# Optimization experiments

Hardware: AMD Instinct MI355X
Metric: run time of the kernel (lower is better)

Reference implementation:

```python
import jax, jax.numpy as jnp
import numpy as np

N_HEAD = 16

def _rope_cos_sin(T, head_dim, dtype):
    # inv_freq over even indices, freqs [T, head_dim//2]
    inv_freq = 1.0 / (10000.0 ** (jnp.arange(0, head_dim, 2, dtype=jnp.float32) / head_dim))
    t = jnp.arange(T, dtype=jnp.float32)
    freqs = t[:, None] * inv_freq[None, :]
    cos = jnp.cos(freqs).astype(dtype)[None, :, None, :]  # [1,T,1,hd/2]
    sin = jnp.sin(freqs).astype(dtype)[None, :, None, :]
    return cos, sin

def _apply_rope(x, cos, sin):
    # x: [B,T,H,hd]; interleaved halves as in the torch module
    x1, x2 = x[..., ::2], x[..., 1::2]
    return jnp.concatenate([x1 * cos - x2 * sin, x1 * sin + x2 * cos], axis=-1)

def setup_inputs() -> dict:
    key = jax.random.key(0)
    k1, k2, k3 = jax.random.split(key, 3)
    B, T, C = 2, 2048, 1024
    x = jax.random.normal(k1, (B, T, C), dtype=jnp.float32)
    # causal mask (mask==0 positions get -inf), broadcast over B and heads
    attn_mask = jnp.tril(jnp.ones((T, T), dtype=bool))[None, None, :, :]
    w_qkv = jax.random.normal(k2, (C, 3 * C), dtype=jnp.float32) * (1.0 / np.sqrt(C))
    w_out = jax.random.normal(k3, (C, C), dtype=jnp.float32) * (1.0 / np.sqrt(C))
    return {"x": x, "attn_mask": attn_mask, "w_qkv": w_qkv, "w_out": w_out}

def reference(x, attn_mask, w_qkv, w_out):
    B, T, C = x.shape
    H = N_HEAD
    hd = C // H
    qkv = x @ w_qkv  # [B,T,3C]
    q, k, v = jnp.split(qkv, 3, axis=2)
    q = q.reshape(B, T, H, hd)
    k = k.reshape(B, T, H, hd)
    v = v.reshape(B, T, H, hd)
    cos, sin = _rope_cos_sin(T, hd, x.dtype)
    q = _apply_rope(q, cos, sin)
    k = _apply_rope(k, cos, sin)
    scale = 1.0 / np.sqrt(hd).astype(np.float32)
    att = jnp.einsum('bthd,bshd->bhts', q, k) * scale  # [B,H,T,T]
    att = jnp.where(attn_mask, att, -jnp.inf)
    att = jax.nn.softmax(att, axis=-1)
    out = jnp.einsum('bhts,bshd->bthd', att, v).reshape(B, T, C)
    out = out @ w_out
    k_t = jnp.transpose(k, (0, 2, 1, 3))  # [B,H,T,hd]
    v_t = jnp.transpose(v, (0, 2, 1, 3))
    return out, k_t, v_t
```

## Files before the change

### kernel.cpp

```cpp
#include <hip/hip_runtime.h>

#define T_SEQ 2048
#define NH    16
#define HD    64
#define CDIM  1024
#define BDIM  2

using floatx4 = __attribute__((ext_vector_type(4))) float;
using bf16x8  = __attribute__((ext_vector_type(8))) __bf16;
using half4   = __attribute__((ext_vector_type(4))) _Float16;
using half8   = __attribute__((ext_vector_type(8))) _Float16;
typedef unsigned short u16;

__device__ __forceinline__ u16 f2bf(float f) {
  unsigned int u = __float_as_uint(f);
  u += 0x7fffu + ((u >> 16) & 1u);
  return (u16)(u >> 16);
}
__device__ __forceinline__ float bf2f(u16 h) {
  return __uint_as_float(((unsigned int)h) << 16);
}
__device__ __forceinline__ u16 f2h(float f) {
  union { _Float16 h; u16 u; } c; c.h = (_Float16)f; return c.u;
}
__device__ __forceinline__ unsigned pk2h(float a, float b) {
  return __builtin_bit_cast(unsigned, __builtin_amdgcn_cvt_pkrtz(a, b));
}
__device__ __forceinline__ void gld16(const void* g, const void* l) {
  __builtin_amdgcn_global_load_lds(
      (const __attribute__((address_space(1))) unsigned int*)(unsigned long long)g,
      (__attribute__((address_space(3))) unsigned int*)(unsigned int)(unsigned long long)l,
      16, 0, 0);
}

__global__ __launch_bounds__(256) void preproc(const float* __restrict__ x,
                                               const float* __restrict__ w_qkv,
                                               const float* __restrict__ w_out,
                                               u16* __restrict__ xb,
                                               u16* __restrict__ wqT,
                                               u16* __restrict__ woT) {
  __shared__ float tile[32][33];
  int blk = blockIdx.x, tid = threadIdx.x;
  if (blk < 4096) {
    int i = blk * 256 + tid;
    float4 v = ((const float4*)x)[i];
    ushort4 o;
    o.x = f2bf(v.x); o.y = f2bf(v.y); o.z = f2bf(v.z); o.w = f2bf(v.w);
    ((ushort4*)xb)[i] = o;
    return;
  }
  const float* W; u16* WT; int K, N, bx, by;
  if (blk < 4096 + 3072) {
    int idx = blk - 4096; W = w_qkv; WT = wqT; K = 1024; N = 3072;
    bx = idx % 96; by = idx / 96;
  } else {
    int idx = blk - 7168; W = w_out; WT = woT; K = 1024; N = 1024;
    bx = idx & 31; by = idx >> 5;
  }
  int n0 = bx * 32, k0 = by * 32;
  int tx = tid & 31, ty = tid >> 5;
#pragma unroll
  for (int i = 0; i < 32; i += 8)
    tile[ty + i][tx] = W[(size_t)(k0 + ty + i) * N + n0 + tx];
  __syncthreads();
#pragma unroll
  for (int i = 0; i < 32; i += 8)
    WT[(size_t)(n0 + ty + i) * K + k0 + tx] = f2bf(tile[tx][ty + i]);
}

template <bool OUT_F32>
__global__ __launch_bounds__(256) void gemm_bt(const u16* __restrict__ A,
                                               const u16* __restrict__ BT,
                                               float* __restrict__ Cf,
                                               u16* __restrict__ Cb,
                                               int M, int N, int K) {
  __shared__ u16 As[2][128 * 32];
  __shared__ u16 Bs[2][128 * 32];
  const int tid  = threadIdx.x;
  const int lane = tid & 63, wave = tid >> 6;
  const int quad = lane >> 4, l16 = lane & 15;
  const int wm = (wave & 1) * 64, wn = (wave >> 1) * 64;
  const int row0 = blockIdx.x * 128, col0 = blockIdx.y * 128;
  const int srow = tid >> 2;
  const int sc   = tid & 3;
  const int sgc  = (sc ^ ((srow >> 1) & 3)) * 8;
  floatx4 acc[4][4] = {};

  auto stage = [&](int buf, int k0) {
    gld16(A  + (size_t)(row0 + srow     ) * K + k0 + sgc, &As[buf][srow * 32 + sc * 8]);
    gld16(A  + (size_t)(row0 + srow + 64) * K + k0 + sgc, &As[buf][(srow + 64) * 32 + sc * 8]);
    gld16(BT + (size_t)(col0 + srow     ) * K + k0 + sgc, &Bs[buf][srow * 32 + sc * 8]);
    gld16(BT + (size_t)(col0 + srow + 64) * K + k0 + sgc, &Bs[buf][(srow + 64) * 32 + sc * 8]);
  };

  const int nk = K >> 5;
  stage(0, 0);
  for (int ki = 0; ki < nk; ki++) {
    const int cur = ki & 1;
    __builtin_amdgcn_s_barrier();
    int kn = ki + 1 < nk ? ki + 1 : nk - 1;
    stage(cur ^ 1, kn << 5);
    asm volatile("s_waitcnt vmcnt(4)" ::: "memory");
    __builtin_amdgcn_s_barrier();
    bf16x8 af[4], bfv[4];
#pragma unroll
    for (int mt = 0; mt < 4; mt++) {
      int r = wm + mt * 16 + l16;
      af[mt] = *(const bf16x8*)&As[cur][r * 32 + (quad ^ ((r >> 1) & 3)) * 8];
    }
#pragma unroll
    for (int nt = 0; nt < 4; nt++) {
      int r = wn + nt * 16 + l16;
      bfv[nt] = *(const bf16x8*)&Bs[cur][r * 32 + (quad ^ ((r >> 1) & 3)) * 8];
    }
#pragma unroll
    for (int mt = 0; mt < 4; mt++)
#pragma unroll
      for (int nt = 0; nt < 4; nt++)
        acc[mt][nt] = __builtin_amdgcn_mfma_f32_16x16x32_bf16(af[mt], bfv[nt], acc[mt][nt], 0, 0, 0);
  }
  asm volatile("s_waitcnt vmcnt(0)" ::: "memory");
#pragma unroll
  for (int mt = 0; mt < 4; mt++)
#pragma unroll
    for (int nt = 0; nt < 4; nt++)
#pragma unroll
      for (int r = 0; r < 4; r++) {
        int row = row0 + wm + mt * 16 + quad * 4 + r;
        int col = col0 + wn + nt * 16 + l16;
        float v = acc[mt][nt][r];
        if (OUT_F32) Cf[(size_t)row * N + col] = v;
        else         Cb[(size_t)row * N + col] = f2bf(v);
      }
}

__global__ __launch_bounds__(256) void rope_vpack(const u16* __restrict__ qkv,
                                                  u16* __restrict__ qf16,
                                                  u16* __restrict__ kf16,
                                                  float* __restrict__ kt_out,
                                                  float* __restrict__ vt_out,
                                                  u16* __restrict__ vtf) {
  int blk = blockIdx.x;
  if (blk < 16384) {
    int gid = blk * 4 + (threadIdx.x >> 6);
    int d   = threadIdx.x & 63;
    int t   = gid & (T_SEQ - 1);
    int h   = (gid >> 11) & 15;
    int b   = gid >> 15;
    const u16* qrow = qkv + ((size_t)(b * T_SEQ + t)) * 3072 + h * 64;
    int i = d & 31;
    unsigned int qp = *(const unsigned int*)(qrow + 2 * i);
    unsigned int kp = *(const unsigned int*)(qrow + 1024 + 2 * i);
    float q1 = bf2f((u16)qp), q2 = bf2f((u16)(qp >> 16));
    float k1 = bf2f((u16)kp), k2 = bf2f((u16)(kp >> 16));
    float inv = expf((float)i * -0.28782313662425572f);
    float ang = (float)t * inv;
    float sn = sinf(ang), cs = cosf(ang);
    float qv = (d < 32) ? (q1 * cs - q2 * sn) : (q1 * sn + q2 * cs);
    float kv = (d < 32) ? (k1 * cs - k2 * sn) : (k1 * sn + k2 * cs);
    size_t o = (size_t)gid * 64 + d;
    qf16[o] = f2h(qv * 0.18033688011112042f);
    kf16[o] = f2h(kv);
    kt_out[o] = kv;
    return;
  }
  __shared__ float tile[64][65];
  int b2 = blk - 16384;
  int t0 = (b2 & 31) * 64;
  int bh = b2 >> 5;
  int b = bh >> 4, h = bh & 15;
  int tx = threadIdx.x & 63, ty = threadIdx.x >> 6;
#pragma unroll
  for (int i = ty; i < 64; i += 4) {
    float v = bf2f(qkv[((size_t)(b * T_SEQ + t0 + i)) * 3072 + 2048 + h * 64 + tx]);
    tile[i][tx] = v;
    vt_out[((size_t)bh * T_SEQ + t0 + i) * 64 + tx] = v;
  }
  __syncthreads();
#pragma unroll
  for (int i = ty; i < 64; i += 4)
    vtf[((size_t)bh * 64 + i) * T_SEQ + t0 + tx] = f2h(tile[tx][i]);
}

__device__ __forceinline__ void qk_dual(const u16* Ks, const half8* qfA, const half8* qfB,
                                        floatx4 (&sA)[8], floatx4 (&sB)[8],
                                        int quad, int l16) {
#pragma unroll
  for (int kc = 0; kc < 2; kc++)
#pragma unroll
    for (int st = 0; st < 8; st++) {
      int srow = st * 16 + l16;
      half8 ak = *(const half8*)&Ks[srow * 64 + (((kc * 4 + quad) ^ (srow & 7)) * 8)];
      sA[st] = __builtin_amdgcn_mfma_f32_16x16x32_f16(ak, qfA[kc], sA[st], 0, 0, 0);
      sB[st] = __builtin_amdgcn_mfma_f32_16x16x32_f16(ak, qfB[kc], sB[st], 0, 0, 0);
    }
}
__device__ __forceinline__ void qk_single(const u16* Ks, const half8* qfA,
                                          floatx4 (&sA)[8], int quad, int l16) {
#pragma unroll
  for (int kc = 0; kc < 2; kc++)
#pragma unroll
    for (int st = 0; st < 8; st++) {
      int srow = st * 16 + l16;
      half8 ak = *(const half8*)&Ks[srow * 64 + (((kc * 4 + quad) ^ (srow & 7)) * 8)];
      sA[st] = __builtin_amdgcn_mfma_f32_16x16x32_f16(ak, qfA[kc], sA[st], 0, 0, 0);
    }
}
__device__ __forceinline__ void apply_mask(floatx4 (&s)[8], int kt, int tw, int quad, int l16) {
  int tg = tw + l16;
#pragma unroll
  for (int st = 0; st < 8; st++) {
    int sg = kt * 128 + st * 16 + quad * 4;
#pragma unroll
    for (int r = 0; r < 4; r++)
      if (sg + r > tg) s[st][r] = -1e30f;
  }
}
__device__ __forceinline__ float vmax4(const floatx4& v) {
  return fmaxf(fmaxf(fmaxf(v[0], v[1]), v[2]), v[3]);
}
__device__ __forceinline__ void softmax_update(floatx4 (&s)[8], float& mrow,
                                               floatx4& lsum, floatx4 (&oacc)[4]) {
  float p0 = fmaxf(vmax4(s[0]), vmax4(s[1]));
  float p1 = fmaxf(vmax4(s[2]), vmax4(s[3]));
  float p2 = fmaxf(vmax4(s[4]), vmax4(s[5]));
  float p3 = fmaxf(vmax4(s[6]), vmax4(s[7]));
  float mx = fmaxf(fmaxf(fmaxf(p0, p1), p2), p3);
  mx = fmaxf(mx, __shfl_xor(mx, 16));
  mx = fmaxf(mx, __shfl_xor(mx, 32));
  if (!__all(mx <= mrow + 8.f)) {
    float mnew = fmaxf(mrow, mx);
    float alpha = exp2f(mrow - mnew);
    mrow = mnew;
    lsum *= alpha;
#pragma unroll
    for (int dt = 0; dt < 4; dt++) oacc[dt] *= alpha;
  }
#pragma unroll
  for (int st = 0; st < 8; st++)
#pragma unroll
    for (int r = 0; r < 4; r++) s[st][r] = exp2f(s[st][r] - mrow);
}
__device__ __forceinline__ void pv_dual(const u16* Vts, const floatx4 (&sA)[8],
                                        const floatx4 (&sB)[8], floatx4 (&oA)[4],
                                        floatx4 (&oB)[4], floatx4& lsA, floatx4& lsB,
                                        int qh2, int ql2, int l16) {
  const half4 vones = {(_Float16)1.f, (_Float16)1.f, (_Float16)1.f, (_Float16)1.f};
#pragma unroll
  for (int st = 0; st < 8; st++) {
    union { unsigned u[2]; half4 h; } pa, pb;
    pa.u[0] = pk2h(sA[st][0], sA[st][1]); pa.u[1] = pk2h(sA[st][2], sA[st][3]);
    pb.u[0] = pk2h(sB[st][0], sB[st][1]); pb.u[1] = pk2h(sB[st][2], sB[st][3]);
    lsA = __builtin_amdgcn_mfma_f32_16x16x16f16(vones, pa.h, lsA, 0, 0, 0);
    lsB = __builtin_amdgcn_mfma_f32_16x16x16f16(vones, pb.h, lsB, 0, 0, 0);
#pragma unroll
    for (int dt = 0; dt < 4; dt++) {
      int drow = dt * 16 + l16;
      half4 av = *(const half4*)&Vts[drow * 128 + (((st * 2 + qh2) ^ (drow & 15)) * 8) + ql2];
      oA[dt] = __builtin_amdgcn_mfma_f32_16x16x16f16(av, pa.h, oA[dt], 0, 0, 0);
      oB[dt] = __builtin_amdgcn_mfma_f32_16x16x16f16(av, pb.h, oB[dt], 0, 0, 0);
    }
  }
}
__device__ __forceinline__ void pv_single(const u16* Vts, const floatx4 (&sA)[8],
                                          floatx4 (&oA)[4], floatx4& lsA,
                                          int qh2, int ql2, int l16) {
  const half4 vones = {(_Float16)1.f, (_Float16)1.f, (_Float16)1.f, (_Float16)1.f};
#pragma unroll
  for (int st = 0; st < 8; st++) {
    union { unsigned u[2]; half4 h; } pa;
    pa.u[0] = pk2h(sA[st][0], sA[st][1]); pa.u[1] = pk2h(sA[st][2], sA[st][3]);
    lsA = __builtin_amdgcn_mfma_f32_16x16x16f16(vones, pa.h, lsA, 0, 0, 0);
#pragma unroll
    for (int dt = 0; dt < 4; dt++) {
      int drow = dt * 16 + l16;
      half4 av = *(const half4*)&Vts[drow * 128 + (((st * 2 + qh2) ^ (drow & 15)) * 8) + ql2];
      oA[dt] = __builtin_amdgcn_mfma_f32_16x16x16f16(av, pa.h, oA[dt], 0, 0, 0);
    }
  }
}
__device__ __forceinline__ void epilogue(u16* __restrict__ Ob, const floatx4 (&oacc)[4],
                                         const floatx4& lsum, int b, int h, int tw,
                                         int quad, int l16) {
  int t = tw + l16;
  float invl = 1.f / lsum[0];
#pragma unroll
  for (int dt = 0; dt < 4; dt++) {
    int d0 = dt * 16 + quad * 4;
    ushort4 o;
    o.x = f2bf(oacc[dt][0] * invl);
    o.y = f2bf(oacc[dt][1] * invl);
    o.z = f2bf(oacc[dt][2] * invl);
    o.w = f2bf(oacc[dt][3] * invl);
    *(ushort4*)&Ob[((size_t)(b * T_SEQ) + t) * CDIM + h * HD + d0] = o;
  }
}

__global__ __launch_bounds__(256, 2) void attn_fused(const u16* __restrict__ qf16,
                                                     const u16* __restrict__ kf16,
                                                     const u16* __restrict__ vtf,
                                                     u16* __restrict__ Ob) {
  __shared__ u16 Ks[128 * 64];
  __shared__ u16 Vts[64 * 128];
  const int tid = threadIdx.x;
  const int lane = tid & 63, wave = tid >> 6;
  const int quad = lane >> 4, l16 = lane & 15;
  const int qh2 = quad >> 1, ql2 = (quad & 1) * 4;
  const int j   = blockIdx.x >> 5;
  const int bh  = blockIdx.x & 31;
  const int b = bh >> 4, h = bh & 15;

  const int qtA = 31 - j, qtB = j;
  const int twA = qtA * 64 + wave * 16;
  const int twB = qtB * 64 + wave * 16;
  const int nktA = (qtA >> 1) + 1;
  const int nktB = (qtB >> 1) + 1;

  const u16* QgA = qf16 + ((size_t)bh * T_SEQ + twA) * HD;
  const u16* QgB = qf16 + ((size_t)bh * T_SEQ + twB) * HD;
  half8 qfA[2], qfB[2];
#pragma unroll
  for (int kc = 0; kc < 2; kc++) {
    qfA[kc] = *(const half8*)&QgA[(size_t)l16 * HD + kc * 32 + quad * 8];
    qfB[kc] = *(const half8*)&QgB[(size_t)l16 * HD + kc * 32 + quad * 8];
  }

  floatx4 oaccA[4] = {}, oaccB[4] = {};
  floatx4 lsA = {}, lsB = {};
  float mA = -1e30f, mB = -1e30f;

#pragma unroll 1
  for (int kt = 0; kt < nktA; kt++) {
    __syncthreads();
    const size_t koff = ((size_t)bh * T_SEQ + kt * 128) * HD;
    const u16* Vg = vtf + (size_t)bh * HD * T_SEQ + kt * 128;
#pragma unroll
    for (int jj = 0; jj < 4; jj++) {
      int t2 = jj * 256 + tid;
      int r = t2 >> 3, c = t2 & 7;
      gld16(kf16 + koff + r * HD + (c ^ (r & 7)) * 8, &Ks[t2 * 8]);
    }
#pragma unroll
    for (int jj = 0; jj < 4; jj++) {
      int t2 = jj * 256 + tid;
      int r = t2 >> 4, c = t2 & 15;
      gld16(Vg + (size_t)r * T_SEQ + (c ^ (r & 15)) * 8, &Vts[t2 * 8]);
    }
    __syncthreads();

    if (kt < nktB) {
      floatx4 sA[8] = {}, sB[8] = {};
      qk_dual(Ks, qfA, qfB, sA, sB, quad, l16);
      if (kt == nktB - 1) apply_mask(sB, kt, twB, quad, l16);
      softmax_update(sA, mA, lsA, oaccA);
      softmax_update(sB, mB, lsB, oaccB);
      pv_dual(Vts, sA, sB, oaccA, oaccB, lsA, lsB, qh2, ql2, l16);
    } else {
      floatx4 sA[8] = {};
      qk_single(Ks, qfA, sA, quad, l16);
      if (kt == nktA - 1) apply_mask(sA, kt, twA, quad, l16);
      softmax_update(sA, mA, lsA, oaccA);
      pv_single(Vts, sA, oaccA, lsA, qh2, ql2, l16);
    }
  }
  epilogue(Ob, oaccA, lsA, b, h, twA, quad, l16);
  epilogue(Ob, oaccB, lsB, b, h, twB, quad, l16);
}

extern "C" void kernel_launch(void* const* d_in, const int* in_sizes, int n_in,
                              void* d_out, int out_size, void* d_ws, size_t ws_size,
                              hipStream_t stream) {
  const float* x     = (const float*)d_in[0];
  const float* w_qkv = (const float*)d_in[2];
  const float* w_out = (const float*)d_in[3];
  float* out    = (float*)d_out;
  float* kt_out = out + (size_t)BDIM * T_SEQ * CDIM;
  float* vt_out = kt_out + (size_t)BDIM * T_SEQ * CDIM;

  const size_t F = (size_t)4194304;
  char* base = (char*)d_ws;
  u16* xb   = (u16*)base;
  u16* wqT  = xb + F;
  u16* woT  = wqT + (size_t)3145728;
  u16* qkvb = woT + (size_t)1048576;
  u16* qf16 = qkvb + (size_t)3 * F;
  u16* kf16 = qf16 + F;
  u16* vtf  = (u16*)base;
  u16* Ob   = kf16 + F;

  preproc<<<8192, 256, 0, stream>>>(x, w_qkv, w_out, xb, wqT, woT);
  gemm_bt<false><<<dim3(32, 24), 256, 0, stream>>>(xb, wqT, (float*)nullptr, qkvb, 4096, 3072, 1024);
  rope_vpack<<<17408, 256, 0, stream>>>(qkvb, qf16, kf16, kt_out, vt_out, vtf);
  attn_fused<<<512, 256, 0, stream>>>(qf16, kf16, vtf, Ob);
  gemm_bt<true><<<dim3(32, 8), 256, 0, stream>>>(Ob, woT, out, (u16*)nullptr, 4096, 1024, 1024);
}
```

Before: 208.3 us.

## Swizzle GEMM block order, halve RoPE threads, hoist attention load pointers

```diff
diff --git a/kernel.cpp b/kernel.cpp
--- a/kernel.cpp
+++ b/kernel.cpp
@@ -80,7 +80,10 @@
   const int lane = tid & 63, wave = tid >> 6;
   const int quad = lane >> 4, l16 = lane & 15;
   const int wm = (wave & 1) * 64, wn = (wave >> 1) * 64;
-  const int row0 = blockIdx.x * 128, col0 = blockIdx.y * 128;
+  const int bid = blockIdx.y * gridDim.x + blockIdx.x;
+  const int cpx = (gridDim.x * gridDim.y) >> 3;
+  const int swz = (bid & 7) * cpx + (bid >> 3);
+  const int row0 = (swz & 31) * 128, col0 = (swz >> 5) * 128;
   const int srow = tid >> 2;
   const int sc   = tid & 3;
   const int sgc  = (sc ^ ((srow >> 1) & 3)) * 8;
@@ -141,31 +144,36 @@
                                                   float* __restrict__ vt_out,
                                                   u16* __restrict__ vtf) {
   int blk = blockIdx.x;
-  if (blk < 16384) {
-    int gid = blk * 4 + (threadIdx.x >> 6);
-    int d   = threadIdx.x & 63;
-    int t   = gid & (T_SEQ - 1);
-    int h   = (gid >> 11) & 15;
-    int b   = gid >> 15;
+  if (blk < 8192) {
+    int rowid = blk * 8 + (threadIdx.x >> 5);
+    int p     = threadIdx.x & 31;
+    int t     = rowid & (T_SEQ - 1);
+    int h     = (rowid >> 11) & 15;
+    int b     = rowid >> 15;
     const u16* qrow = qkv + ((size_t)(b * T_SEQ + t)) * 3072 + h * 64;
-    int i = d & 31;
-    unsigned int qp = *(const unsigned int*)(qrow + 2 * i);
-    unsigned int kp = *(const unsigned int*)(qrow + 1024 + 2 * i);
+    unsigned int qp = *(const unsigned int*)(qrow + 2 * p);
+    unsigned int kp = *(const unsigned int*)(qrow + 1024 + 2 * p);
     float q1 = bf2f((u16)qp), q2 = bf2f((u16)(qp >> 16));
     float k1 = bf2f((u16)kp), k2 = bf2f((u16)(kp >> 16));
-    float inv = expf((float)i * -0.28782313662425572f);
-    float ang = (float)t * inv;
-    float sn = sinf(ang), cs = cosf(ang);
-    float qv = (d < 32) ? (q1 * cs - q2 * sn) : (q1 * sn + q2 * cs);
-    float kv = (d < 32) ? (k1 * cs - k2 * sn) : (k1 * sn + k2 * cs);
-    size_t o = (size_t)gid * 64 + d;
-    qf16[o] = f2h(qv * 0.18033688011112042f);
-    kf16[o] = f2h(kv);
-    kt_out[o] = kv;
+    float inv_rev = exp2f(-0.4152410118609203f * (float)p) * 0.15915494309189535f;
+    float rev = (float)t * inv_rev;
+    float fr  = rev - floorf(rev);
+    float sn = __builtin_amdgcn_sinf(fr);
+    float cs = __builtin_amdgcn_cosf(fr);
+    float qv1 = q1 * cs - q2 * sn, qv2 = q1 * sn + q2 * cs;
+    float kv1 = k1 * cs - k2 * sn, kv2 = k1 * sn + k2 * cs;
+    size_t o = (size_t)rowid * 64;
+    const float s = 0.18033688011112042f;
+    qf16[o + p]      = f2h(qv1 * s);
+    qf16[o + p + 32] = f2h(qv2 * s);
+    kf16[o + p]      = f2h(kv1);
+    kf16[o + p + 32] = f2h(kv2);
+    kt_out[o + p]      = kv1;
+    kt_out[o + p + 32] = kv2;
     return;
   }
   __shared__ float tile[64][65];
-  int b2 = blk - 16384;
+  int b2 = blk - 8192;
   int t0 = (b2 & 31) * 64;
   int bh = b2 >> 5;
   int b = bh >> 4, h = bh & 15;
@@ -325,6 +333,19 @@
     qfB[kc] = *(const half8*)&QgB[(size_t)l16 * HD + kc * 32 + quad * 8];
   }
 
+  const u16* kp_[4]; const u16* vp_[4];
+  u16* kl_[4]; u16* vl_[4];
+#pragma unroll
+  for (int jj = 0; jj < 4; jj++) {
+    int t2 = jj * 256 + tid;
+    int r = t2 >> 3, c = t2 & 7;
+    kp_[jj] = kf16 + ((size_t)bh * T_SEQ) * HD + r * HD + (c ^ (r & 7)) * 8;
+    kl_[jj] = &Ks[t2 * 8];
+    int r2 = t2 >> 4, c2 = t2 & 15;
+    vp_[jj] = vtf + (size_t)bh * HD * T_SEQ + (size_t)r2 * T_SEQ + (c2 ^ (r2 & 15)) * 8;
+    vl_[jj] = &Vts[t2 * 8];
+  }
+
   floatx4 oaccA[4] = {}, oaccB[4] = {};
   floatx4 lsA = {}, lsB = {};
   float mA = -1e30f, mB = -1e30f;
@@ -332,21 +353,13 @@
 #pragma unroll 1
   for (int kt = 0; kt < nktA; kt++) {
     __syncthreads();
-    const size_t koff = ((size_t)bh * T_SEQ + kt * 128) * HD;
-    const u16* Vg = vtf + (size_t)bh * HD * T_SEQ + kt * 128;
-#pragma unroll
-    for (int jj = 0; jj < 4; jj++) {
-      int t2 = jj * 256 + tid;
-      int r = t2 >> 3, c = t2 & 7;
-      gld16(kf16 + koff + r * HD + (c ^ (r & 7)) * 8, &Ks[t2 * 8]);
-    }
-#pragma unroll
-    for (int jj = 0; jj < 4; jj++) {
-      int t2 = jj * 256 + tid;
-      int r = t2 >> 4, c = t2 & 15;
-      gld16(Vg + (size_t)r * T_SEQ + (c ^ (r & 15)) * 8, &Vts[t2 * 8]);
-    }
+#pragma unroll
+    for (int jj = 0; jj < 4; jj++) gld16(kp_[jj], kl_[jj]);
+#pragma unroll
+    for (int jj = 0; jj < 4; jj++) gld16(vp_[jj], vl_[jj]);
     __syncthreads();
+#pragma unroll
+    for (int jj = 0; jj < 4; jj++) { kp_[jj] += 128 * HD; vp_[jj] += 128; }
 
     if (kt < nktB) {
       floatx4 sA[8] = {}, sB[8] = {};
@@ -390,7 +403,7 @@
 
   preproc<<<8192, 256, 0, stream>>>(x, w_qkv, w_out, xb, wqT, woT);
   gemm_bt<false><<<dim3(32, 24), 256, 0, stream>>>(xb, wqT, (float*)nullptr, qkvb, 4096, 3072, 1024);
-  rope_vpack<<<17408, 256, 0, stream>>>(qkvb, qf16, kf16, kt_out, vt_out, vtf);
+  rope_vpack<<<9216, 256, 0, stream>>>(qkvb, qf16, kf16, kt_out, vt_out, vtf);
   attn_fused<<<512, 256, 0, stream>>>(qf16, kf16, vtf, Ob);
   gemm_bt<true><<<dim3(32, 8), 256, 0, stream>>>(Ob, woT, out, (u16*)nullptr, 4096, 1024, 1024);
 }
```

New measurement: 212.0 us. No clear change (+1.8%).
